# Kernel optimization log

Measured on AMD Instinct MI355X. Metric: run time of the kernel, lower is better.

The kernel has to match this reference:

```python
import jax, jax.numpy as jnp
import numpy as np

D_MODEL = 1024
D_FF = 4096
NUM_EXPERTS = 8
TOP_K = 2
LB_COEF = 0.01
Z_COEF = 0.001
EPS_LN = 1e-5


def setup_inputs() -> dict:
    key = jax.random.key(0)
    ks = jax.random.split(key, 8)
    B, L = 4, 2048
    s_in = 1.0 / np.sqrt(D_MODEL)
    s_ff = 1.0 / np.sqrt(D_FF)
    return {
        "x": jax.random.normal(ks[0], (B, L, D_MODEL), dtype=jnp.float32),
        "gate_w": jax.random.normal(ks[1], (NUM_EXPERTS, D_MODEL), dtype=jnp.float32) * s_in,
        "ln_g": jnp.ones((D_MODEL,), dtype=jnp.float32),
        "ln_b": jnp.zeros((D_MODEL,), dtype=jnp.float32),
        "w1": jax.random.normal(ks[2], (NUM_EXPERTS, D_MODEL, D_FF), dtype=jnp.float32) * s_in,
        "b1": jnp.zeros((NUM_EXPERTS, D_FF), dtype=jnp.float32),
        "w2": jax.random.normal(ks[3], (NUM_EXPERTS, D_FF, D_MODEL), dtype=jnp.float32) * s_ff,
        "b2": jnp.zeros((NUM_EXPERTS, D_MODEL), dtype=jnp.float32),
    }


def reference(x, gate_w, ln_g, ln_b, w1, b1, w2, b2):
    B, L, D = x.shape
    xf = x.reshape(-1, D)  # [T, D]

    # LayerNorm
    mu = jnp.mean(xf, axis=-1, keepdims=True)
    var = jnp.mean((xf - mu) ** 2, axis=-1, keepdims=True)
    x_norm = (xf - mu) * jax.lax.rsqrt(var + EPS_LN) * ln_g + ln_b

    # Router (eval mode: no noise)
    logits = jnp.clip(x_norm @ gate_w.T, -10.0, 10.0)  # [T, E]
    z_loss = jnp.mean(jax.nn.logsumexp(logits, axis=-1) ** 2) * Z_COEF
    probs = jax.nn.softmax(logits, axis=-1)

    gw, idx = jax.lax.top_k(probs, TOP_K)  # [T, K]
    gw = gw / (jnp.sum(gw, axis=-1, keepdims=True) + 1e-8)

    # Load-balancing aux loss uses top-1 assignment
    top1_mask = jax.nn.one_hot(idx[:, 0], NUM_EXPERTS, dtype=jnp.float32)
    fraction_routed = jnp.mean(top1_mask, axis=0)
    mean_prob = jnp.mean(probs, axis=0)
    aux_loss = NUM_EXPERTS * jnp.sum(fraction_routed * mean_prob) * LB_COEF
    total_aux = aux_loss + z_loss

    # Combine weights [T, E]: sum over k of gate weight where routed to e
    combine = jnp.einsum("tk,tke->te", gw, jax.nn.one_hot(idx, NUM_EXPERTS, dtype=gw.dtype))

    # Dense per-expert FFN (Expert: Linear -> GELU -> Linear), combined by weights
    out = jnp.zeros_like(xf)
    for e in range(NUM_EXPERTS):
        h = jax.nn.gelu(x_norm @ w1[e] + b1[e], approximate=False)
        y = h @ w2[e] + b2[e]
        out = out + combine[:, e:e + 1] * y

    return x + out.reshape(B, L, D), total_aux
```

## Files before the change

kernel.cpp:

```cpp
#include <hip/hip_runtime.h>
#include <math.h>

typedef __bf16 bf16_t;
typedef bf16_t bf16x8 __attribute__((ext_vector_type(8)));
typedef bf16_t bf16x4 __attribute__((ext_vector_type(4)));
typedef float  f32x4  __attribute__((ext_vector_type(4)));

#define T_TOK 8192
#define DM 1024
#define DF 4096
#define NE 8
#define NP 16384

__device__ __forceinline__ f32x4 mfma_bf16(bf16x8 a, bf16x8 b, f32x4 c) {
  return __builtin_amdgcn_mfma_f32_16x16x32_bf16(a, b, c, 0, 0, 0);
}

__device__ __forceinline__ void gload16(const void* g, void* l) {
  __builtin_amdgcn_global_load_lds((const __attribute__((address_space(1))) void*)g,
                                   (__attribute__((address_space(3))) void*)l, 16, 0, 0);
}

__device__ __forceinline__ float erf_fast(float x) {
  float ax = fabsf(x);
  float t = 1.f / (1.f + 0.3275911f * ax);
  float p = t * (0.254829592f + t * (-0.284496736f + t * (1.421413741f +
            t * (-1.453152027f + t * 1.061405429f))));
  float r = 1.f - p * __expf(-ax * ax);
  return copysignf(r, x);
}

__device__ __forceinline__ unsigned swz_off(int row, int ch) {
  return (unsigned)(((row >> 1) << 7) + (((((row & 1) << 2) | ch) ^ ((row >> 1) & 7)) << 4));
}


__global__ __launch_bounds__(256) void k_router(
    const float* __restrict__ x, const float* __restrict__ gate_w,
    const float* __restrict__ ln_g, const float* __restrict__ ln_b,
    float* __restrict__ out, bf16_t* __restrict__ xn,
    int* __restrict__ eidx, float* __restrict__ gts, int* __restrict__ meta)
{
  int* cnt1 = meta;
  int* cnt2 = meta + 8;
  float* probsum = (float*)(meta + 32);
  float* zsum    = (float*)(meta + 40);

  __shared__ float sprob[8];
  __shared__ float sz;
  __shared__ int sc1[8], sc2[8];
  if (threadIdx.x < 8) { sprob[threadIdx.x] = 0.f; sc1[threadIdx.x] = 0; sc2[threadIdx.x] = 0; }
  if (threadIdx.x == 8) sz = 0.f;
  __syncthreads();

  int lane = threadIdx.x & 63, wv = threadIdx.x >> 6;
  int t = blockIdx.x * 4 + wv;
  const float* xt = x + (size_t)t * DM;

  float4 v[4];
  float s1 = 0.f, s2 = 0.f;
  #pragma unroll
  for (int c = 0; c < 4; ++c) {
    v[c] = *(const float4*)(xt + c * 256 + lane * 4);
    s1 += v[c].x + v[c].y + v[c].z + v[c].w;
    s2 += v[c].x * v[c].x + v[c].y * v[c].y + v[c].z * v[c].z + v[c].w * v[c].w;
  }
  #pragma unroll
  for (int o = 32; o > 0; o >>= 1) { s1 += __shfl_xor(s1, o, 64); s2 += __shfl_xor(s2, o, 64); }
  float mu = s1 * (1.f / DM);
  float var = s2 * (1.f / DM) - mu * mu;
  float rstd = rsqrtf(var + 1e-5f);

  float xv[16];
  #pragma unroll
  for (int c = 0; c < 4; ++c) {
    int d = c * 256 + lane * 4;
    float4 g4 = *(const float4*)(ln_g + d);
    float4 b4 = *(const float4*)(ln_b + d);
    xv[c*4+0] = (v[c].x - mu) * rstd * g4.x + b4.x;
    xv[c*4+1] = (v[c].y - mu) * rstd * g4.y + b4.y;
    xv[c*4+2] = (v[c].z - mu) * rstd * g4.z + b4.z;
    xv[c*4+3] = (v[c].w - mu) * rstd * g4.w + b4.w;
    *(float4*)(out + (size_t)t * DM + d) = v[c];
    bf16x4 pk = { (bf16_t)xv[c*4+0], (bf16_t)xv[c*4+1], (bf16_t)xv[c*4+2], (bf16_t)xv[c*4+3] };
    *(bf16x4*)(xn + (size_t)t * DM + d) = pk;
  }

  float lg[8];
  #pragma unroll
  for (int e = 0; e < 8; ++e) {
    float p = 0.f;
    #pragma unroll
    for (int c = 0; c < 4; ++c) {
      int d = c * 256 + lane * 4;
      float4 g4 = *(const float4*)(gate_w + e * DM + d);
      p += xv[c*4+0] * g4.x + xv[c*4+1] * g4.y + xv[c*4+2] * g4.z + xv[c*4+3] * g4.w;
    }
    #pragma unroll
    for (int o = 32; o > 0; o >>= 1) p += __shfl_xor(p, o, 64);
    lg[e] = p;
  }

  if (lane == 0) {
    float m = -1e30f;
    #pragma unroll
    for (int e = 0; e < 8; ++e) { lg[e] = fminf(fmaxf(lg[e], -10.f), 10.f); m = fmaxf(m, lg[e]); }
    float pr[8]; float se = 0.f;
    #pragma unroll
    for (int e = 0; e < 8; ++e) { pr[e] = expf(lg[e] - m); se += pr[e]; }
    float inv = 1.f / se;
    #pragma unroll
    for (int e = 0; e < 8; ++e) pr[e] *= inv;
    float lse = m + logf(se);

    int e0 = 0; float p0 = pr[0];
    #pragma unroll
    for (int e = 1; e < 8; ++e) if (pr[e] > p0) { p0 = pr[e]; e0 = e; }
    int e1 = -1; float p1 = -1.f;
    #pragma unroll
    for (int e = 0; e < 8; ++e) if (e != e0 && pr[e] > p1) { p1 = pr[e]; e1 = e; }
    float s = p0 + p1 + 1e-8f;
    eidx[t*2]   = e0; eidx[t*2+1] = e1;
    gts[t*2]    = p0 / s; gts[t*2+1] = p1 / s;

    atomicAdd(&sc1[e0], 1);
    atomicAdd(&sc2[e0], 1);
    atomicAdd(&sc2[e1], 1);
    #pragma unroll
    for (int e = 0; e < 8; ++e) atomicAdd(&sprob[e], pr[e]);
    atomicAdd(&sz, lse * lse);
  }
  __syncthreads();
  if (threadIdx.x < 8) {
    if (sc1[threadIdx.x]) atomicAdd(&cnt1[threadIdx.x], sc1[threadIdx.x]);
    if (sc2[threadIdx.x]) atomicAdd(&cnt2[threadIdx.x], sc2[threadIdx.x]);
    atomicAdd(&probsum[threadIdx.x], sprob[threadIdx.x]);
  }
  if (threadIdx.x == 8) atomicAdd(zsum, sz);
}

__global__ __launch_bounds__(256) void k_convT(
    const float* __restrict__ src, bf16_t* __restrict__ dst, int R, int C)
{
  __shared__ float tile[64][65];
  int e = blockIdx.z;
  const float* s = src + (size_t)e * R * C;
  bf16_t* d = dst + (size_t)e * R * C;
  int c0 = blockIdx.x * 64, r0 = blockIdx.y * 64;
  int t = threadIdx.x;
  #pragma unroll
  for (int i = 0; i < 4; ++i) {
    int idx = i * 256 + t;
    int r = idx >> 4, c4 = (idx & 15) * 4;
    float4 v = *(const float4*)(s + (size_t)(r0 + r) * C + c0 + c4);
    tile[r][c4]   = v.x; tile[r][c4+1] = v.y;
    tile[r][c4+2] = v.z; tile[r][c4+3] = v.w;
  }
  __syncthreads();
  #pragma unroll
  for (int i = 0; i < 2; ++i) {
    int idx = i * 256 + t;
    int c = idx >> 3, r8 = (idx & 7) * 8;
    bf16x8 pk;
    #pragma unroll
    for (int k = 0; k < 8; ++k) pk[k] = (bf16_t)tile[r8 + k][c];
    *(bf16x8*)(d + (size_t)(c0 + c) * R + r0 + r8) = pk;
  }
}

__global__ void k_finalize(int* __restrict__ meta, float* __restrict__ aux_out) {
  if (threadIdx.x == 0 && blockIdx.x == 0) {
    int acc = 0;
    for (int e = 0; e < 8; ++e) { meta[24 + e] = acc; acc += meta[8 + e]; }
    const float* probsum = (const float*)(meta + 32);
    const float* zsum    = (const float*)(meta + 40);
    float s = 0.f;
    for (int e = 0; e < 8; ++e)
      s += ((float)meta[e] * (1.f / 8192.f)) * (probsum[e] * (1.f / 8192.f));
    aux_out[0] = 8.f * s * 0.01f + (zsum[0] * (1.f / 8192.f)) * 0.001f;
  }
}

__global__ __launch_bounds__(256) void k_assign(
    const int* __restrict__ eidx, float* __restrict__ gts,
    int* __restrict__ meta, int* __restrict__ list, float* __restrict__ gl,
    int* __restrict__ t2s)
{
  int t = blockIdx.x * 256 + threadIdx.x;
  int* cursor = meta + 16;
  const int* off = meta + 24;
  #pragma unroll
  for (int k = 0; k < 2; ++k) {
    int e = eidx[t*2 + k];
    float g = gts[t*2 + k];
    int pos = atomicAdd(&cursor[e], 1);
    int slot = off[e] + pos;
    list[slot] = t;
    gl[slot] = g;
    t2s[t*2 + k] = slot;
  }
}


#define STAGE1(KT, BO) do { \
  _Pragma("unroll") for (int r = 0; r < 2; ++r) gload16(sA[r] + (KT) * 32, smem + (BO) + dA[r]); \
  _Pragma("unroll") for (int r = 0; r < 4; ++r) gload16(sB[r] + (KT) * 32, smem + (BO) + dB[r]); \
} while (0)

#define COMPUTE1(BO) do { \
  bf16x8 bfr[4]; \
  _Pragma("unroll") for (int j = 0; j < 4; ++j) bfr[j] = *(const bf16x8*)(smem + (BO) + b_off[j]); \
  _Pragma("unroll") for (int i = 0; i < 8; ++i) { \
    bf16x8 af = *(const bf16x8*)(smem + (BO) + a_off[i]); \
    _Pragma("unroll") for (int j = 0; j < 4; ++j) acc[i][j] = mfma_bf16(af, bfr[j], acc[i][j]); \
  } \
} while (0)

__global__ __launch_bounds__(256, 2) void k_ffn1(
    const bf16_t* __restrict__ xn, const bf16_t* __restrict__ w1t,
    const float* __restrict__ b1, bf16_t* __restrict__ H,
    const int* __restrict__ list, const int* __restrict__ meta)
{
  int e = blockIdx.z;
  int cnt = meta[8 + e];
  int m0 = blockIdx.y * 128;
  if (m0 >= cnt) return;
  int offe = meta[24 + e];
  int n0 = blockIdx.x * 256;

  __shared__ __align__(1024) char smem[49152];
  int tid = threadIdx.x, lane = tid & 63, wv = tid >> 6;

  const bf16_t* sA[2]; const bf16_t* sB[4];
  unsigned dA[2], dB[4];
  #pragma unroll
  for (int i = 0; i < 2; ++i) {
    int s = i * 256 + tid;
    int line = s >> 3, u = s & 7, w = u ^ (line & 7);
    int row = (line << 1) | (w >> 2), ch = w & 3;
    int mrow = min(m0 + row, cnt - 1);
    int token = list[offe + mrow];
    sA[i] = xn + (size_t)token * DM + ch * 8;
    dA[i] = (unsigned)(i * 4096 + wv * 1024);
  }
  #pragma unroll
  for (int i = 0; i < 4; ++i) {
    int s = i * 256 + tid;
    int line = s >> 3, u = s & 7, w = u ^ (line & 7);
    int row = (line << 1) | (w >> 2), ch = w & 3;
    sB[i] = w1t + ((size_t)e * DF + n0 + row) * DM + ch * 8;
    dB[i] = (unsigned)(8192 + i * 4096 + wv * 1024);
  }

  unsigned a_off[8], b_off[4];
  #pragma unroll
  for (int i = 0; i < 8; ++i) a_off[i] = swz_off(i * 16 + (lane & 15), lane >> 4);
  #pragma unroll
  for (int j = 0; j < 4; ++j) b_off[j] = 8192u + swz_off(wv * 64 + j * 16 + (lane & 15), lane >> 4);

  f32x4 acc[8][4];
  #pragma unroll
  for (int i = 0; i < 8; ++i)
    #pragma unroll
    for (int j = 0; j < 4; ++j)
      acc[i][j] = (f32x4){0.f, 0.f, 0.f, 0.f};

  STAGE1(0, 0);
  __syncthreads();
  for (int kt = 0; kt < DM / 32; kt += 2) {
    STAGE1(kt + 1, 24576);
    COMPUTE1(0);
    __syncthreads();
    if (kt + 2 < DM / 32) STAGE1(kt + 2, 0);
    COMPUTE1(24576);
    __syncthreads();
  }

  int rq = (lane >> 4) << 2;
  int cbase = n0 + wv * 64 + (lane & 15);
  #pragma unroll
  for (int i = 0; i < 8; ++i) {
    #pragma unroll
    for (int q = 0; q < 4; ++q) {
      int mg = m0 + i * 16 + rq + q;
      if (mg < cnt) {
        size_t hrow = (size_t)(offe + mg) * DF;
        #pragma unroll
        for (int j = 0; j < 4; ++j) {
          int col = cbase + j * 16;
          float hv = acc[i][j][q] + b1[e * DF + col];
          hv = 0.5f * hv * (1.f + erf_fast(hv * 0.70710678118f));
          H[hrow + col] = (bf16_t)hv;
        }
      }
    }
  }
}

__global__ __launch_bounds__(256, 2) void k_ffn2(
    const bf16_t* __restrict__ H, const bf16_t* __restrict__ w2t,
    const float* __restrict__ b2, bf16_t* __restrict__ Y,
    const int* __restrict__ meta)
{
  int e = blockIdx.z;
  int cnt = meta[8 + e];
  int m0 = blockIdx.y * 128;
  if (m0 >= cnt) return;
  int offe = meta[24 + e];
  int n0 = blockIdx.x * 256;

  __shared__ __align__(1024) char smem[49152];
  int tid = threadIdx.x, lane = tid & 63, wv = tid >> 6;

  const bf16_t* sA[2]; const bf16_t* sB[4];
  unsigned dA[2], dB[4];
  #pragma unroll
  for (int i = 0; i < 2; ++i) {
    int s = i * 256 + tid;
    int line = s >> 3, u = s & 7, w = u ^ (line & 7);
    int row = (line << 1) | (w >> 2), ch = w & 3;
    int mrow = min(m0 + row, cnt - 1);
    sA[i] = H + (size_t)(offe + mrow) * DF + ch * 8;
    dA[i] = (unsigned)(i * 4096 + wv * 1024);
  }
  #pragma unroll
  for (int i = 0; i < 4; ++i) {
    int s = i * 256 + tid;
    int line = s >> 3, u = s & 7, w = u ^ (line & 7);
    int row = (line << 1) | (w >> 2), ch = w & 3;
    sB[i] = w2t + ((size_t)e * DM + n0 + row) * DF + ch * 8;
    dB[i] = (unsigned)(8192 + i * 4096 + wv * 1024);
  }

  unsigned a_off[8], b_off[4];
  #pragma unroll
  for (int i = 0; i < 8; ++i) a_off[i] = swz_off(i * 16 + (lane & 15), lane >> 4);
  #pragma unroll
  for (int j = 0; j < 4; ++j) b_off[j] = 8192u + swz_off(wv * 64 + j * 16 + (lane & 15), lane >> 4);

  f32x4 acc[8][4];
  #pragma unroll
  for (int i = 0; i < 8; ++i)
    #pragma unroll
    for (int j = 0; j < 4; ++j)
      acc[i][j] = (f32x4){0.f, 0.f, 0.f, 0.f};

  STAGE1(0, 0);
  __syncthreads();
  for (int kt = 0; kt < DF / 32; kt += 2) {
    STAGE1(kt + 1, 24576);
    COMPUTE1(0);
    __syncthreads();
    if (kt + 2 < DF / 32) STAGE1(kt + 2, 0);
    COMPUTE1(24576);
    __syncthreads();
  }

  int rq = (lane >> 4) << 2;
  int cbase = n0 + wv * 64 + (lane & 15);
  #pragma unroll
  for (int i = 0; i < 8; ++i) {
    #pragma unroll
    for (int q = 0; q < 4; ++q) {
      int mg = m0 + i * 16 + rq + q;
      if (mg < cnt) {
        size_t yrow = (size_t)(offe + mg) * DM;
        #pragma unroll
        for (int j = 0; j < 4; ++j) {
          int col = cbase + j * 16;
          Y[yrow + col] = (bf16_t)(acc[i][j][q] + b2[e * DM + col]);
        }
      }
    }
  }
}

__global__ __launch_bounds__(256) void k_combine(
    const bf16_t* __restrict__ Y, const int* __restrict__ t2s,
    const float* __restrict__ gl, float* __restrict__ out)
{
  int lane = threadIdx.x & 63, wv = threadIdx.x >> 6;
  int t = blockIdx.x * 4 + wv;
  int s0 = t2s[t*2], s1 = t2s[t*2 + 1];
  float g0 = gl[s0], g1 = gl[s1];
  const bf16_t* y0 = Y + (size_t)s0 * DM;
  const bf16_t* y1 = Y + (size_t)s1 * DM;
  float* o = out + (size_t)t * DM;
  #pragma unroll
  for (int c = 0; c < 4; ++c) {
    int d = c * 256 + lane * 4;
    float4 r  = *(const float4*)(o + d);
    bf16x4 a = *(const bf16x4*)(y0 + d);
    bf16x4 b = *(const bf16x4*)(y1 + d);
    r.x += g0 * (float)a[0] + g1 * (float)b[0];
    r.y += g0 * (float)a[1] + g1 * (float)b[1];
    r.z += g0 * (float)a[2] + g1 * (float)b[2];
    r.w += g0 * (float)a[3] + g1 * (float)b[3];
    *(float4*)(o + d) = r;
  }
}

extern "C" void kernel_launch(void* const* d_in, const int* in_sizes, int n_in,
                              void* d_out, int out_size, void* d_ws, size_t ws_size,
                              hipStream_t stream) {
  const float* x      = (const float*)d_in[0];
  const float* gate_w = (const float*)d_in[1];
  const float* ln_g   = (const float*)d_in[2];
  const float* ln_b   = (const float*)d_in[3];
  const float* w1     = (const float*)d_in[4];
  const float* b1     = (const float*)d_in[5];
  const float* w2     = (const float*)d_in[6];
  const float* b2     = (const float*)d_in[7];
  float* out = (float*)d_out;

  char* ws = (char*)d_ws;
  bf16_t* xn   = (bf16_t*)(ws);
  bf16_t* w1t  = (bf16_t*)(ws + 16777216ull);
  bf16_t* Y    = (bf16_t*)(ws + 16777216ull);
  bf16_t* w2t  = (bf16_t*)(ws + 83886080ull);
  bf16_t* H    = (bf16_t*)(ws + 150994944ull);
  int*    list = (int*)   (ws + 285212672ull);
  float*  gl   = (float*) (ws + 285278208ull);
  int*    eidx = (int*)   (ws + 285343744ull);
  float*  gts  = (float*) (ws + 285409280ull);
  int*    t2s  = (int*)   (ws + 285409280ull);
  int*    meta = (int*)   (ws + 285474816ull);

  hipMemsetAsync(meta, 0, 256, stream);
  k_router<<<T_TOK / 4, 256, 0, stream>>>(x, gate_w, ln_g, ln_b, out, xn, eidx, gts, meta);
  k_convT<<<dim3(DF / 64, DM / 64, NE), 256, 0, stream>>>(w1, w1t, DM, DF);
  k_convT<<<dim3(DM / 64, DF / 64, NE), 256, 0, stream>>>(w2, w2t, DF, DM);
  k_finalize<<<1, 1, 0, stream>>>(meta, out + (size_t)T_TOK * DM);
  k_assign<<<T_TOK / 256, 256, 0, stream>>>(eidx, gts, meta, list, gl, t2s);
  k_ffn1<<<dim3(DF / 256, 64, NE), 256, 0, stream>>>(xn, w1t, b1, H, list, meta);
  k_ffn2<<<dim3(DM / 256, 64, NE), 256, 0, stream>>>(H, w2t, b2, Y, meta);
  k_combine<<<T_TOK / 4, 256, 0, stream>>>(Y, t2s, gl, out);
}
```

Baseline: 686.8 us.

## Use partial vmcnt waits and setprio in GEMM k-loop; merge weight transposes

The double-buffered k-loop in both FFN GEMMs replaces __syncthreads with explicit s_waitcnt vmcnt(6) plus s_barrier, so only the older stage's async LDS loads are awaited while the next stage's loads stay in flight. It also raises wave priority around the MFMA compute block. Separately, the two weight-transpose/convert launches are merged into one 1D-grid kernel to save a launch. The hand-counted vmcnt assumes exactly six outstanding loads per stage, which is fragile if the staging code changes.

```diff
diff --git a/kernel.cpp b/kernel.cpp
--- a/kernel.cpp
+++ b/kernel.cpp
@@ -139,14 +139,25 @@
   if (threadIdx.x == 8) atomicAdd(zsum, sz);
 }
 
-__global__ __launch_bounds__(256) void k_convT(
-    const float* __restrict__ src, bf16_t* __restrict__ dst, int R, int C)
-{
+__global__ __launch_bounds__(256) void k_convT2(
+    const float* __restrict__ w1, bf16_t* __restrict__ w1t,
+    const float* __restrict__ w2, bf16_t* __restrict__ w2t)
+{
+  int bid = blockIdx.x;
+  const float* s; bf16_t* d; int R, C, c0, r0;
+  if (bid < 8192) {
+    int e = bid >> 10, rem = bid & 1023;
+    R = DM; C = DF;
+    s = w1 + (size_t)e * R * C; d = w1t + (size_t)e * R * C;
+    c0 = (rem & 63) * 64; r0 = (rem >> 6) * 64;
+  } else {
+    int e = (bid - 8192) >> 10, rem = (bid - 8192) & 1023;
+    R = DF; C = DM;
+    s = w2 + (size_t)e * R * C; d = w2t + (size_t)e * R * C;
+    c0 = (rem & 15) * 64; r0 = (rem >> 4) * 64;
+  }
+
   __shared__ float tile[64][65];
-  int e = blockIdx.z;
-  const float* s = src + (size_t)e * R * C;
-  bf16_t* d = dst + (size_t)e * R * C;
-  int c0 = blockIdx.x * 64, r0 = blockIdx.y * 64;
   int t = threadIdx.x;
   #pragma unroll
   for (int i = 0; i < 4; ++i) {
@@ -216,6 +227,36 @@
   } \
 } while (0)
 
+#define WAITV6 do { __builtin_amdgcn_sched_barrier(0); \
+  asm volatile("s_waitcnt vmcnt(6)" ::: "memory"); \
+  __builtin_amdgcn_sched_barrier(0); __builtin_amdgcn_s_barrier(); \
+  __builtin_amdgcn_sched_barrier(0); } while (0)
+
+#define WAITV0 do { __builtin_amdgcn_sched_barrier(0); \
+  asm volatile("s_waitcnt vmcnt(0)" ::: "memory"); \
+  __builtin_amdgcn_sched_barrier(0); __builtin_amdgcn_s_barrier(); \
+  __builtin_amdgcn_sched_barrier(0); } while (0)
+
+#define ENDBAR do { __builtin_amdgcn_sched_barrier(0); \
+  __builtin_amdgcn_s_barrier(); __builtin_amdgcn_sched_barrier(0); } while (0)
+
+#define KLOOP(NT) do { \
+  STAGE1(0, 0); \
+  for (int kt = 0; kt < (NT); kt += 2) { \
+    STAGE1(kt + 1, 24576); \
+    WAITV6; \
+    __builtin_amdgcn_s_setprio(1); \
+    COMPUTE1(0); \
+    __builtin_amdgcn_s_setprio(0); \
+    ENDBAR; \
+    if (kt + 2 < (NT)) { STAGE1(kt + 2, 0); WAITV6; } else { WAITV0; } \
+    __builtin_amdgcn_s_setprio(1); \
+    COMPUTE1(24576); \
+    __builtin_amdgcn_s_setprio(0); \
+    ENDBAR; \
+  } \
+} while (0)
+
 __global__ __launch_bounds__(256, 2) void k_ffn1(
     const bf16_t* __restrict__ xn, const bf16_t* __restrict__ w1t,
     const float* __restrict__ b1, bf16_t* __restrict__ H,
@@ -265,16 +306,7 @@
     for (int j = 0; j < 4; ++j)
       acc[i][j] = (f32x4){0.f, 0.f, 0.f, 0.f};
 
-  STAGE1(0, 0);
-  __syncthreads();
-  for (int kt = 0; kt < DM / 32; kt += 2) {
-    STAGE1(kt + 1, 24576);
-    COMPUTE1(0);
-    __syncthreads();
-    if (kt + 2 < DM / 32) STAGE1(kt + 2, 0);
-    COMPUTE1(24576);
-    __syncthreads();
-  }
+  KLOOP(DM / 32);
 
   int rq = (lane >> 4) << 2;
   int cbase = n0 + wv * 64 + (lane & 15);
@@ -345,16 +377,7 @@
     for (int j = 0; j < 4; ++j)
       acc[i][j] = (f32x4){0.f, 0.f, 0.f, 0.f};
 
-  STAGE1(0, 0);
-  __syncthreads();
-  for (int kt = 0; kt < DF / 32; kt += 2) {
-    STAGE1(kt + 1, 24576);
-    COMPUTE1(0);
-    __syncthreads();
-    if (kt + 2 < DF / 32) STAGE1(kt + 2, 0);
-    COMPUTE1(24576);
-    __syncthreads();
-  }
+  KLOOP(DF / 32);
 
   int rq = (lane >> 4) << 2;
   int cbase = n0 + wv * 64 + (lane & 15);
@@ -428,8 +451,7 @@
 
   hipMemsetAsync(meta, 0, 256, stream);
   k_router<<<T_TOK / 4, 256, 0, stream>>>(x, gate_w, ln_g, ln_b, out, xn, eidx, gts, meta);
-  k_convT<<<dim3(DF / 64, DM / 64, NE), 256, 0, stream>>>(w1, w1t, DM, DF);
-  k_convT<<<dim3(DM / 64, DF / 64, NE), 256, 0, stream>>>(w2, w2t, DF, DM);
+  k_convT2<<<16384, 256, 0, stream>>>(w1, w1t, w2, w2t);
   k_finalize<<<1, 1, 0, stream>>>(meta, out + (size_t)T_TOK * DM);
   k_assign<<<T_TOK / 256, 256, 0, stream>>>(eidx, gts, meta, list, gl, t2s);
   k_ffn1<<<dim3(DF / 256, 64, NE), 256, 0, stream>>>(xn, w1t, b1, H, list, meta);
```

Measured after the change: 685.5 us. Within noise of the previous version (-0.2%).
